# Kernel optimization log

Hardware: AMD Instinct MI355X
Metric: run time of the kernel (lower is better)

The kernel has to match this reference:

```python
import jax, jax.numpy as jnp
import numpy as np

WS = 8
NH = 6

def _ln(x, g, b, eps=1e-5):
    m = jnp.mean(x, axis=-1, keepdims=True)
    v = jnp.var(x, axis=-1, keepdims=True)
    return (x - m) * jax.lax.rsqrt(v + eps) * g + b

def setup_inputs() -> dict:
    key = jax.random.key(0)
    ks = jax.random.split(key, 6)
    B, H, W, C = 4, 256, 256, 192
    s = 0.02
    return {
        "x": jax.random.normal(ks[0], (B, H, W, C), jnp.float32),
        "g1": jnp.ones((C,), jnp.float32),
        "b1": jnp.zeros((C,), jnp.float32),
        "w_qkv": jax.random.normal(ks[1], (C, 3 * C), jnp.float32) * s,
        "b_qkv": jnp.zeros((3 * C,), jnp.float32),
        "w_proj": jax.random.normal(ks[2], (C, C), jnp.float32) * s,
        "b_proj": jnp.zeros((C,), jnp.float32),
        "g2": jnp.ones((C,), jnp.float32),
        "b2": jnp.zeros((C,), jnp.float32),
        "w_fc1": jax.random.normal(ks[3], (C, 4 * C), jnp.float32) * s,
        "b_fc1": jnp.zeros((4 * C,), jnp.float32),
        "w_fc2": jax.random.normal(ks[4], (4 * C, C), jnp.float32) * s,
        "b_fc2": jnp.zeros((C,), jnp.float32),
    }

def reference(x, g1, b1, w_qkv, b_qkv, w_proj, b_proj, g2, b2, w_fc1, b_fc1, w_fc2, b_fc2):
    B, H, W, C = x.shape
    ws, nh = WS, NH
    hd = C // nh
    scale = hd ** -0.5
    N = ws * ws
    # window partition: (B,H,W,C) -> (B*nW, N, C). H,W divisible by ws, so pad branch is a no-op.
    xw = x.reshape(B, H // ws, ws, W // ws, ws, C).transpose(0, 1, 3, 2, 4, 5).reshape(-1, N, C)
    h = _ln(xw, g1, b1)
    qkv = h @ w_qkv + b_qkv                      # (Bn, N, 3C)
    q, k, v = jnp.split(qkv, 3, axis=-1)
    q = q.reshape(-1, N, nh, hd)
    k = k.reshape(-1, N, nh, hd)
    v = v.reshape(-1, N, nh, hd)
    attn = jax.nn.softmax(jnp.einsum('bnhd,bmhd->bhnm', q, k) * scale, axis=-1)
    o = jnp.einsum('bhnm,bmhd->bnhd', attn, v).reshape(-1, N, C)
    xw = xw + (o @ w_proj + b_proj)              # residual inside windows
    # window unpartition: (B*nW, N, C) -> (B, H, W, C)
    xo = xw.reshape(B, H // ws, W // ws, ws, ws, C).transpose(0, 1, 3, 2, 4, 5).reshape(B, H, W, C)
    h2 = _ln(xo, g2, b2)
    h2 = jax.nn.gelu(h2 @ w_fc1 + b_fc1, approximate=False) @ w_fc2 + b_fc2
    return xo + h2
```

## Files before the change

kernel.cpp:

```cpp
#include <hip/hip_runtime.h>
#include <hip/hip_bf16.h>

typedef unsigned short u16;
typedef __attribute__((ext_vector_type(8))) short short8;
typedef __attribute__((ext_vector_type(4))) short short4v;
typedef __attribute__((ext_vector_type(4))) float f32x4;

#define TOK 262144

__device__ __forceinline__ u16 f2bf(float f){
  __hip_bfloat16 h = __float2bfloat16(f);
  return *reinterpret_cast<u16*>(&h);
}

__device__ __forceinline__ float gelu_fast(float u){
  float uu = u * u;
  float e = __expf(u * fmaf(uu, -0.0713548163f, -1.5957691216f));
  return u * __builtin_amdgcn_rcpf(1.f + e);
}

__global__ void transpose_all(const float* __restrict__ w0, u16* __restrict__ d0,
                              const float* __restrict__ w1, u16* __restrict__ d1,
                              const float* __restrict__ w2, u16* __restrict__ d2,
                              const float* __restrict__ w3, u16* __restrict__ d3)
{
  int seg = blockIdx.y;
  const float* s; u16* d; int K, N;
  if      (seg == 0){ s = w0; d = d0; K = 192; N = 576; }
  else if (seg == 1){ s = w1; d = d1; K = 192; N = 192; }
  else if (seg == 2){ s = w2; d = d2; K = 192; N = 768; }
  else              { s = w3; d = d3; K = 768; N = 192; }
  int idx = blockIdx.x * 256 + threadIdx.x;
  if (idx < K * N){
    int k = idx / N, n = idx % N;
    d[n * K + k] = f2bf(s[idx]);
  }
}

__global__ __launch_bounds__(256, 2) void win_attn(
    const float* __restrict__ x,  const float* __restrict__ g1, const float* __restrict__ b1,
    const u16* __restrict__ wqkvT, const float* __restrict__ bqkv,
    const u16* __restrict__ wprojT, const float* __restrict__ bproj,
    float* __restrict__ out)
{
  __shared__ u16 hw[64 * 200];
  __shared__ u16 wch[96 * 200];
  u16* Ql = wch;
  u16* Kl = wch + 64 * 40;
  u16* Vt = Kl  + 64 * 40;
  u16* Pl = Vt  + 32 * 72;

  const int tid = threadIdx.x, lane = tid & 63, w = tid >> 6;
  const int l15 = lane & 15, quad = lane >> 4;
  const int wid = blockIdx.x;
  const int b = wid >> 10, hy = (wid >> 5) & 31, wx = wid & 31;

  {
    int n = w * 16 + (lane >> 2), p = lane & 3;
    int hr = hy * 8 + (n >> 3), wcc = wx * 8 + (n & 7);
    size_t tg = ((size_t)(b * 256 + hr)) * 256 + wcc;
    const float* xr = x + tg * 192 + p * 48;
    float v[48];
    #pragma unroll
    for (int c = 0; c < 12; c++) *(float4*)(v + c * 4) = *(const float4*)(xr + c * 4);
    float s = 0.f, ss = 0.f;
    #pragma unroll
    for (int i = 0; i < 48; i++){ s += v[i]; ss += v[i] * v[i]; }
    s += __shfl_xor(s, 1); ss += __shfl_xor(ss, 1);
    s += __shfl_xor(s, 2); ss += __shfl_xor(ss, 2);
    float m  = s * (1.f / 192.f);
    float rs = rsqrtf(ss * (1.f / 192.f) - m * m + 1e-5f);
    #pragma unroll
    for (int c = 0; c < 12; c++){
      float4 gv = *(const float4*)(g1 + p * 48 + c * 4);
      float4 bv = *(const float4*)(b1 + p * 48 + c * 4);
      short4v t;
      t.x = (short)f2bf((v[c*4+0] - m) * rs * gv.x + bv.x);
      t.y = (short)f2bf((v[c*4+1] - m) * rs * gv.y + bv.y);
      t.z = (short)f2bf((v[c*4+2] - m) * rs * gv.z + bv.z);
      t.w = (short)f2bf((v[c*4+3] - m) * rs * gv.w + bv.w);
      *(short4v*)&hw[n * 200 + p * 48 + c * 4] = t;
    }
  }

  const int qrow = w * 16 + quad * 4;
  f32x4 oall[6][2];
  #pragma unroll
  for (int h = 0; h < 6; h++)
    #pragma unroll
    for (int nt = 0; nt < 2; nt++) oall[h][nt] = (f32x4){0.f, 0.f, 0.f, 0.f};

  #pragma unroll
  for (int head = 0; head < 6; ++head){
    __syncthreads();
    #pragma unroll
    for (int it = 0; it < 9; ++it){
      int c = tid + it * 256;
      int row = c / 24, cc = c % 24;
      int gr = (row >> 5) * 192 + head * 32 + (row & 31);
      *(uint4*)&wch[row * 200 + cc * 8] = *(const uint4*)(wqkvT + (size_t)gr * 192 + cc * 8);
    }
    __syncthreads();
    f32x4 acc[3][2];
    #pragma unroll
    for (int mat = 0; mat < 3; mat++)
      #pragma unroll
      for (int nt = 0; nt < 2; nt++) acc[mat][nt] = (f32x4){0.f, 0.f, 0.f, 0.f};
    #pragma unroll
    for (int k = 0; k < 6; k++){
      short8 af = *(const short8*)&hw[(w * 16 + l15) * 200 + k * 32 + quad * 8];
      #pragma unroll
      for (int mat = 0; mat < 3; mat++)
        #pragma unroll
        for (int nt = 0; nt < 2; nt++){
          short8 bfv = *(const short8*)&wch[(mat * 32 + nt * 16 + l15) * 200 + k * 32 + quad * 8];
          acc[mat][nt] = __builtin_amdgcn_mfma_f32_16x16x32_bf16(af, bfv, acc[mat][nt], 0, 0, 0);
        }
    }
    __syncthreads();
    #pragma unroll
    for (int nt = 0; nt < 2; nt++){
      float bq = bqkv[      head * 32 + nt * 16 + l15];
      float bk = bqkv[192 + head * 32 + nt * 16 + l15];
      float bv = bqkv[384 + head * 32 + nt * 16 + l15];
      #pragma unroll
      for (int r = 0; r < 4; r++){
        Ql[(qrow + r) * 40 + nt * 16 + l15] = f2bf(acc[0][nt][r] + bq);
        Kl[(qrow + r) * 40 + nt * 16 + l15] = f2bf(acc[1][nt][r] + bk);
        Vt[(nt * 16 + l15) * 72 + qrow + r] = f2bf(acc[2][nt][r] + bv);
      }
    }
    __syncthreads();
    short8 aq = *(const short8*)&Ql[(w * 16 + l15) * 40 + quad * 8];
    f32x4 sa[4];
    #pragma unroll
    for (int kt = 0; kt < 4; kt++){
      short8 bk8 = *(const short8*)&Kl[(kt * 16 + l15) * 40 + quad * 8];
      sa[kt] = __builtin_amdgcn_mfma_f32_16x16x32_bf16(aq, bk8, (f32x4){0.f,0.f,0.f,0.f}, 0, 0, 0);
    }
    const float scale = 0.17677669529663687f;
    float inv[4];
    #pragma unroll
    for (int r = 0; r < 4; r++){
      float s0 = sa[0][r] * scale, s1 = sa[1][r] * scale;
      float s2 = sa[2][r] * scale, s3 = sa[3][r] * scale;
      float mx = fmaxf(fmaxf(s0, s1), fmaxf(s2, s3));
      mx = fmaxf(mx, __shfl_xor(mx, 1)); mx = fmaxf(mx, __shfl_xor(mx, 2));
      mx = fmaxf(mx, __shfl_xor(mx, 4)); mx = fmaxf(mx, __shfl_xor(mx, 8));
      float p0 = __expf(s0 - mx), p1 = __expf(s1 - mx);
      float p2 = __expf(s2 - mx), p3 = __expf(s3 - mx);
      float l = p0 + p1 + p2 + p3;
      l += __shfl_xor(l, 1); l += __shfl_xor(l, 2);
      l += __shfl_xor(l, 4); l += __shfl_xor(l, 8);
      inv[r] = 1.f / l;
      Pl[(qrow + r) * 72 +      l15] = f2bf(p0);
      Pl[(qrow + r) * 72 + 16 + l15] = f2bf(p1);
      Pl[(qrow + r) * 72 + 32 + l15] = f2bf(p2);
      Pl[(qrow + r) * 72 + 48 + l15] = f2bf(p3);
    }
    f32x4 oa[2];
    oa[0] = (f32x4){0.f,0.f,0.f,0.f}; oa[1] = (f32x4){0.f,0.f,0.f,0.f};
    #pragma unroll
    for (int ks = 0; ks < 2; ks++){
      short8 ap = *(const short8*)&Pl[(w * 16 + l15) * 72 + ks * 32 + quad * 8];
      #pragma unroll
      for (int nt = 0; nt < 2; nt++){
        short8 bv8 = *(const short8*)&Vt[(nt * 16 + l15) * 72 + ks * 32 + quad * 8];
        oa[nt] = __builtin_amdgcn_mfma_f32_16x16x32_bf16(ap, bv8, oa[nt], 0, 0, 0);
      }
    }
    #pragma unroll
    for (int nt = 0; nt < 2; nt++)
      #pragma unroll
      for (int r = 0; r < 4; r++)
        oall[head][nt][r] = oa[nt][r] * inv[r];
  }

  #pragma unroll
  for (int h = 0; h < 6; h++)
    #pragma unroll
    for (int nt = 0; nt < 2; nt++)
      #pragma unroll
      for (int r = 0; r < 4; r++)
        hw[(qrow + r) * 200 + h * 32 + nt * 16 + l15] = f2bf(oall[h][nt][r]);

  f32x4 accP[12];
  #pragma unroll
  for (int nt = 0; nt < 12; nt++) accP[nt] = (f32x4){0.f,0.f,0.f,0.f};
  #pragma unroll
  for (int k = 0; k < 6; k++){
    short8 af = *(const short8*)&hw[(w * 16 + l15) * 200 + k * 32 + quad * 8];
    #pragma unroll
    for (int nt = 0; nt < 12; nt++){
      short8 bfv = *(const short8*)(wprojT + (size_t)(nt * 16 + l15) * 192 + k * 32 + quad * 8);
      accP[nt] = __builtin_amdgcn_mfma_f32_16x16x32_bf16(af, bfv, accP[nt], 0, 0, 0);
    }
  }
  #pragma unroll
  for (int r = 0; r < 4; r++){
    int nn = qrow + r;
    int hr = hy * 8 + (nn >> 3), wcc = wx * 8 + (nn & 7);
    size_t tg = ((size_t)(b * 256 + hr)) * 256 + wcc;
    #pragma unroll
    for (int nt = 0; nt < 12; nt++){
      int col = nt * 16 + l15;
      size_t idx = tg * 192 + col;
      out[idx] = accP[nt][r] + bproj[col] + x[idx];
    }
  }
}

__global__ __launch_bounds__(256, 2) void mlp_fused(
    const float* __restrict__ g2, const float* __restrict__ b2,
    const u16* __restrict__ wfc1T, const float* __restrict__ bfc1,
    const u16* __restrict__ wfc2T, const float* __restrict__ bfc2,
    float* __restrict__ io)
{
  __shared__ u16 h2t[64 * 200];
  __shared__ u16 w1b[32 * 200];
  __shared__ u16 w2b[192 * 40];
  __shared__ u16 Ut [64 * 40];

  const int tid = threadIdx.x, lane = tid & 63, w = tid >> 6;
  const int l15 = lane & 15, quad = lane >> 4;
  const int t0 = blockIdx.x * 64;

  const int c0 = tid, c1 = tid + 256, c2 = tid + 512;
  const int w1r0 = c0 / 24, w1c0 = c0 % 24;
  const int w1r1 = c1 / 24, w1c1 = c1 % 24;
  const int w1r2 = c2 / 24, w1c2 = c2 % 24;
  const int w2r0 = c0 >> 2, w2c0 = c0 & 3;
  const int w2r1 = c1 >> 2, w2c1 = c1 & 3;
  const int w2r2 = c2 >> 2, w2c2 = c2 & 3;

  uint4 r1a, r1b, r1c, r2a, r2b, r2c;
  r1a = *(const uint4*)(wfc1T + (size_t)w1r0 * 192 + w1c0 * 8);
  r1b = *(const uint4*)(wfc1T + (size_t)w1r1 * 192 + w1c1 * 8);
  r1c = *(const uint4*)(wfc1T + (size_t)w1r2 * 192 + w1c2 * 8);
  r2a = *(const uint4*)(wfc2T + (size_t)w2r0 * 768 + w2c0 * 8);
  r2b = *(const uint4*)(wfc2T + (size_t)w2r1 * 768 + w2c1 * 8);
  r2c = *(const uint4*)(wfc2T + (size_t)w2r2 * 768 + w2c2 * 8);

  {
    int n = w * 16 + (lane >> 2), p = lane & 3;
    const float* xr = io + (size_t)(t0 + n) * 192 + p * 48;
    float v[48];
    #pragma unroll
    for (int c = 0; c < 12; c++) *(float4*)(v + c * 4) = *(const float4*)(xr + c * 4);
    float s = 0.f, ss = 0.f;
    #pragma unroll
    for (int i = 0; i < 48; i++){ s += v[i]; ss += v[i] * v[i]; }
    s += __shfl_xor(s, 1); ss += __shfl_xor(ss, 1);
    s += __shfl_xor(s, 2); ss += __shfl_xor(ss, 2);
    float m  = s * (1.f / 192.f);
    float rs = rsqrtf(ss * (1.f / 192.f) - m * m + 1e-5f);
    #pragma unroll
    for (int c = 0; c < 12; c++){
      float4 gv = *(const float4*)(g2 + p * 48 + c * 4);
      float4 bv = *(const float4*)(b2 + p * 48 + c * 4);
      short4v t;
      t.x = (short)f2bf((v[c*4+0] - m) * rs * gv.x + bv.x);
      t.y = (short)f2bf((v[c*4+1] - m) * rs * gv.y + bv.y);
      t.z = (short)f2bf((v[c*4+2] - m) * rs * gv.z + bv.z);
      t.w = (short)f2bf((v[c*4+3] - m) * rs * gv.w + bv.w);
      *(short4v*)&h2t[n * 200 + p * 48 + c * 4] = t;
    }
  }

  f32x4 accO[12];
  #pragma unroll
  for (int nt = 0; nt < 12; nt++) accO[nt] = (f32x4){0.f,0.f,0.f,0.f};

  for (int ch = 0; ch < 24; ++ch){
    *(uint4*)&w1b[w1r0 * 200 + w1c0 * 8] = r1a;
    *(uint4*)&w1b[w1r1 * 200 + w1c1 * 8] = r1b;
    *(uint4*)&w1b[w1r2 * 200 + w1c2 * 8] = r1c;
    *(uint4*)&w2b[w2r0 * 40 + w2c0 * 8] = r2a;
    *(uint4*)&w2b[w2r1 * 40 + w2c1 * 8] = r2b;
    *(uint4*)&w2b[w2r2 * 40 + w2c2 * 8] = r2c;
    if (ch < 23){
      int chn = ch + 1;
      r1a = *(const uint4*)(wfc1T + (size_t)(chn * 32 + w1r0) * 192 + w1c0 * 8);
      r1b = *(const uint4*)(wfc1T + (size_t)(chn * 32 + w1r1) * 192 + w1c1 * 8);
      r1c = *(const uint4*)(wfc1T + (size_t)(chn * 32 + w1r2) * 192 + w1c2 * 8);
      r2a = *(const uint4*)(wfc2T + (size_t)w2r0 * 768 + chn * 32 + w2c0 * 8);
      r2b = *(const uint4*)(wfc2T + (size_t)w2r1 * 768 + chn * 32 + w2c1 * 8);
      r2c = *(const uint4*)(wfc2T + (size_t)w2r2 * 768 + chn * 32 + w2c2 * 8);
    }
    __syncthreads();

    f32x4 au[2];
    au[0] = (f32x4){0.f,0.f,0.f,0.f}; au[1] = (f32x4){0.f,0.f,0.f,0.f};
    #pragma unroll
    for (int k = 0; k < 6; k++){
      short8 af = *(const short8*)&h2t[(w * 16 + l15) * 200 + k * 32 + quad * 8];
      #pragma unroll
      for (int nt = 0; nt < 2; nt++){
        short8 bfv = *(const short8*)&w1b[(nt * 16 + l15) * 200 + k * 32 + quad * 8];
        au[nt] = __builtin_amdgcn_mfma_f32_16x16x32_bf16(af, bfv, au[nt], 0, 0, 0);
      }
    }
    #pragma unroll
    for (int nt = 0; nt < 2; nt++){
      float bb = bfc1[ch * 32 + nt * 16 + l15];
      #pragma unroll
      for (int r = 0; r < 4; r++){
        float u = au[nt][r] + bb;
        Ut[(w * 16 + quad * 4 + r) * 40 + nt * 16 + l15] = f2bf(gelu_fast(u));
      }
    }
    short8 auf = *(const short8*)&Ut[(w * 16 + l15) * 40 + quad * 8];
    #pragma unroll
    for (int nt = 0; nt < 12; nt++){
      short8 bfv = *(const short8*)&w2b[(nt * 16 + l15) * 40 + quad * 8];
      accO[nt] = __builtin_amdgcn_mfma_f32_16x16x32_bf16(auf, bfv, accO[nt], 0, 0, 0);
    }
    __syncthreads();
  }

  #pragma unroll
  for (int nt = 0; nt < 12; nt++){
    int col = nt * 16 + l15;
    float bb = bfc2[col];
    #pragma unroll
    for (int r = 0; r < 4; r++){
      int row = t0 + w * 16 + quad * 4 + r;
      size_t idx = (size_t)row * 192 + col;
      io[idx] = accO[nt][r] + bb + io[idx];
    }
  }
}

extern "C" void kernel_launch(void* const* d_in, const int* in_sizes, int n_in,
                              void* d_out, int out_size, void* d_ws, size_t ws_size,
                              hipStream_t stream) {
  const float* x      = (const float*)d_in[0];
  const float* g1     = (const float*)d_in[1];
  const float* b1     = (const float*)d_in[2];
  const float* w_qkv  = (const float*)d_in[3];
  const float* b_qkv  = (const float*)d_in[4];
  const float* w_proj = (const float*)d_in[5];
  const float* b_proj = (const float*)d_in[6];
  const float* g2     = (const float*)d_in[7];
  const float* b2     = (const float*)d_in[8];
  const float* w_fc1  = (const float*)d_in[9];
  const float* b_fc1  = (const float*)d_in[10];
  const float* w_fc2  = (const float*)d_in[11];
  const float* b_fc2  = (const float*)d_in[12];
  float* out = (float*)d_out;

  u16* wqkvT  = (u16*)d_ws;
  u16* wprojT = wqkvT  + 576 * 192;
  u16* wfc1T  = wprojT + 192 * 192;
  u16* wfc2T  = wfc1T  + 768 * 192;

  transpose_all<<<dim3(576, 4), 256, 0, stream>>>(w_qkv, wqkvT, w_proj, wprojT,
                                                  w_fc1, wfc1T, w_fc2, wfc2T);
  win_attn<<<4096, 256, 0, stream>>>(x, g1, b1, wqkvT, b_qkv, wprojT, b_proj, out);
  mlp_fused<<<4096, 256, 0, stream>>>(g2, b2, wfc1T, b_fc1, wfc2T, b_fc2, out);
}
```

Baseline: 973.4 us.

## Swizzle LDS tiles with XOR layout and prefetch next head's QKV weights

Replaces the padded 200-element LDS row stride with a 192-stride XOR-swizzled layout for the activation and weight tiles in both kernels. This is meant to avoid bank conflicts while using less shared memory. The attention kernel also prefetches the next head's QKV weight slice into registers while the current head computes, so global load latency overlaps with MFMA work. The cost is nine extra uint4 registers per thread, which adds register pressure and could reduce occupancy.

```diff
diff --git a/kernel.cpp b/kernel.cpp
--- a/kernel.cpp
+++ b/kernel.cpp
@@ -6,8 +6,6 @@
 typedef __attribute__((ext_vector_type(4))) short short4v;
 typedef __attribute__((ext_vector_type(4))) float f32x4;
 
-#define TOK 262144
-
 __device__ __forceinline__ u16 f2bf(float f){
   __hip_bfloat16 h = __float2bfloat16(f);
   return *reinterpret_cast<u16*>(&h);
@@ -17,6 +15,10 @@
   float uu = u * u;
   float e = __expf(u * fmaf(uu, -0.0713548163f, -1.5957691216f));
   return u * __builtin_amdgcn_rcpf(1.f + e);
+}
+
+__device__ __forceinline__ int swz(int row, int col){
+  return row * 192 + (col ^ ((row & 7) << 3));
 }
 
 __global__ void transpose_all(const float* __restrict__ w0, u16* __restrict__ d0,
@@ -43,8 +45,8 @@
     const u16* __restrict__ wprojT, const float* __restrict__ bproj,
     float* __restrict__ out)
 {
-  __shared__ u16 hw[64 * 200];
-  __shared__ u16 wch[96 * 200];
+  __shared__ u16 hw[64 * 192];
+  __shared__ u16 wch[96 * 192];
   u16* Ql = wch;
   u16* Kl = wch + 64 * 40;
   u16* Vt = Kl  + 64 * 40;
@@ -54,6 +56,18 @@
   const int l15 = lane & 15, quad = lane >> 4;
   const int wid = blockIdx.x;
   const int b = wid >> 10, hy = (wid >> 5) & 31, wx = wid & 31;
+
+  int srow[9], scc[9], sbase[9];
+  #pragma unroll
+  for (int it = 0; it < 9; ++it){
+    int c = tid + it * 256;
+    srow[it] = c / 24; scc[it] = c % 24;
+    sbase[it] = (srow[it] >> 5) * 192 + (srow[it] & 31);
+  }
+  uint4 pre[9];
+  #pragma unroll
+  for (int it = 0; it < 9; ++it)
+    pre[it] = *(const uint4*)(wqkvT + (size_t)sbase[it] * 192 + scc[it] * 8);
 
   {
     int n = w * 16 + (lane >> 2), p = lane & 3;
@@ -79,7 +93,7 @@
       t.y = (short)f2bf((v[c*4+1] - m) * rs * gv.y + bv.y);
       t.z = (short)f2bf((v[c*4+2] - m) * rs * gv.z + bv.z);
       t.w = (short)f2bf((v[c*4+3] - m) * rs * gv.w + bv.w);
-      *(short4v*)&hw[n * 200 + p * 48 + c * 4] = t;
+      *(short4v*)&hw[swz(n, p * 48 + c * 4)] = t;
     }
   }
 
@@ -94,11 +108,12 @@
   for (int head = 0; head < 6; ++head){
     __syncthreads();
     #pragma unroll
-    for (int it = 0; it < 9; ++it){
-      int c = tid + it * 256;
-      int row = c / 24, cc = c % 24;
-      int gr = (row >> 5) * 192 + head * 32 + (row & 31);
-      *(uint4*)&wch[row * 200 + cc * 8] = *(const uint4*)(wqkvT + (size_t)gr * 192 + cc * 8);
+    for (int it = 0; it < 9; ++it)
+      *(uint4*)&wch[swz(srow[it], scc[it] * 8)] = pre[it];
+    if (head < 5){
+      #pragma unroll
+      for (int it = 0; it < 9; ++it)
+        pre[it] = *(const uint4*)(wqkvT + (size_t)(sbase[it] + (head + 1) * 32) * 192 + scc[it] * 8);
     }
     __syncthreads();
     f32x4 acc[3][2];
@@ -108,12 +123,12 @@
       for (int nt = 0; nt < 2; nt++) acc[mat][nt] = (f32x4){0.f, 0.f, 0.f, 0.f};
     #pragma unroll
     for (int k = 0; k < 6; k++){
-      short8 af = *(const short8*)&hw[(w * 16 + l15) * 200 + k * 32 + quad * 8];
+      short8 af = *(const short8*)&hw[swz(w * 16 + l15, k * 32 + quad * 8)];
       #pragma unroll
       for (int mat = 0; mat < 3; mat++)
         #pragma unroll
         for (int nt = 0; nt < 2; nt++){
-          short8 bfv = *(const short8*)&wch[(mat * 32 + nt * 16 + l15) * 200 + k * 32 + quad * 8];
+          short8 bfv = *(const short8*)&wch[swz(mat * 32 + nt * 16 + l15, k * 32 + quad * 8)];
           acc[mat][nt] = __builtin_amdgcn_mfma_f32_16x16x32_bf16(af, bfv, acc[mat][nt], 0, 0, 0);
         }
     }
@@ -182,14 +197,14 @@
     for (int nt = 0; nt < 2; nt++)
       #pragma unroll
       for (int r = 0; r < 4; r++)
-        hw[(qrow + r) * 200 + h * 32 + nt * 16 + l15] = f2bf(oall[h][nt][r]);
+        hw[swz(qrow + r, h * 32 + nt * 16 + l15)] = f2bf(oall[h][nt][r]);
 
   f32x4 accP[12];
   #pragma unroll
   for (int nt = 0; nt < 12; nt++) accP[nt] = (f32x4){0.f,0.f,0.f,0.f};
   #pragma unroll
   for (int k = 0; k < 6; k++){
-    short8 af = *(const short8*)&hw[(w * 16 + l15) * 200 + k * 32 + quad * 8];
+    short8 af = *(const short8*)&hw[swz(w * 16 + l15, k * 32 + quad * 8)];
     #pragma unroll
     for (int nt = 0; nt < 12; nt++){
       short8 bfv = *(const short8*)(wprojT + (size_t)(nt * 16 + l15) * 192 + k * 32 + quad * 8);
@@ -216,8 +231,8 @@
     const u16* __restrict__ wfc2T, const float* __restrict__ bfc2,
     float* __restrict__ io)
 {
-  __shared__ u16 h2t[64 * 200];
-  __shared__ u16 w1b[32 * 200];
+  __shared__ u16 h2t[64 * 192];
+  __shared__ u16 w1b[32 * 192];
   __shared__ u16 w2b[192 * 40];
   __shared__ u16 Ut [64 * 40];
 
@@ -263,7 +278,7 @@
       t.y = (short)f2bf((v[c*4+1] - m) * rs * gv.y + bv.y);
       t.z = (short)f2bf((v[c*4+2] - m) * rs * gv.z + bv.z);
       t.w = (short)f2bf((v[c*4+3] - m) * rs * gv.w + bv.w);
-      *(short4v*)&h2t[n * 200 + p * 48 + c * 4] = t;
+      *(short4v*)&h2t[swz(n, p * 48 + c * 4)] = t;
     }
   }
 
@@ -272,9 +287,9 @@
   for (int nt = 0; nt < 12; nt++) accO[nt] = (f32x4){0.f,0.f,0.f,0.f};
 
   for (int ch = 0; ch < 24; ++ch){
-    *(uint4*)&w1b[w1r0 * 200 + w1c0 * 8] = r1a;
-    *(uint4*)&w1b[w1r1 * 200 + w1c1 * 8] = r1b;
-    *(uint4*)&w1b[w1r2 * 200 + w1c2 * 8] = r1c;
+    *(uint4*)&w1b[swz(w1r0, w1c0 * 8)] = r1a;
+    *(uint4*)&w1b[swz(w1r1, w1c1 * 8)] = r1b;
+    *(uint4*)&w1b[swz(w1r2, w1c2 * 8)] = r1c;
     *(uint4*)&w2b[w2r0 * 40 + w2c0 * 8] = r2a;
     *(uint4*)&w2b[w2r1 * 40 + w2c1 * 8] = r2b;
     *(uint4*)&w2b[w2r2 * 40 + w2c2 * 8] = r2c;
@@ -293,10 +308,10 @@
     au[0] = (f32x4){0.f,0.f,0.f,0.f}; au[1] = (f32x4){0.f,0.f,0.f,0.f};
     #pragma unroll
     for (int k = 0; k < 6; k++){
-      short8 af = *(const short8*)&h2t[(w * 16 + l15) * 200 + k * 32 + quad * 8];
+      short8 af = *(const short8*)&h2t[swz(w * 16 + l15, k * 32 + quad * 8)];
       #pragma unroll
       for (int nt = 0; nt < 2; nt++){
-        short8 bfv = *(const short8*)&w1b[(nt * 16 + l15) * 200 + k * 32 + quad * 8];
+        short8 bfv = *(const short8*)&w1b[swz(nt * 16 + l15, k * 32 + quad * 8)];
         au[nt] = __builtin_amdgcn_mfma_f32_16x16x32_bf16(af, bfv, au[nt], 0, 0, 0);
       }
     }
```

New measurement: 1.113 ms. 14.3% more time.
